# Kernel optimization log

Hardware: AMD Instinct MI355X
Metric: run time of the kernel (lower is better)

Reference implementation:

```python
import jax, jax.numpy as jnp
import numpy as np

N = 20000
NUM_CLASSES = 30


def setup_inputs() -> dict:
    key = jax.random.key(0)
    k1, k2, k3 = jax.random.split(key, 3)
    mean_3d = jax.random.normal(k1, (N, 3), dtype=jnp.float32)
    mean_3d_cano = jax.random.normal(k2, (N, 3), dtype=jnp.float32)
    segm_labels = jax.random.randint(k3, (N,), 0, NUM_CLASSES, dtype=jnp.int32)
    return {"mean_3d": mean_3d, "mean_3d_cano": mean_3d_cano, "segm_labels": segm_labels}


def reference(mean_3d, mean_3d_cano, segm_labels):
    # Brute-force K=1 nearest neighbor: squared euclidean distance
    # d2[i, j] = ||x_i||^2 - 2 x_i . y_j + ||y_j||^2  -> [N, N]
    x2 = jnp.sum(mean_3d * mean_3d, axis=-1, keepdims=True)          # [N, 1]
    y2 = jnp.sum(mean_3d_cano * mean_3d_cano, axis=-1)               # [N]
    d2 = x2 - 2.0 * (mean_3d @ mean_3d_cano.T) + y2[None, :]         # [N, N]
    nearest_ids = jnp.argmin(d2, axis=1)                              # [N]
    matched_labels = segm_labels[nearest_ids]
    semantic_inconsistent = (matched_labels != segm_labels)
    semantic_loss = semantic_inconsistent.astype(jnp.float32).mean()
    return semantic_loss
```

## Files before the change

### kernel.cpp

```cpp
#include <hip/hip_runtime.h>

#define N_PTS 20000
#define NA 20480
#define NB 20032
#define TILES_TOTAL 640
#define A_BYTES  (NA * 16 * 2)
#define B_BYTES  (NB * 16 * 2)
#define BEST_OFF (A_BYTES + B_BYTES)
#define CNT_OFF  (BEST_OFF + NB * 8)

typedef __attribute__((ext_vector_type(8))) short bf16x8;
typedef __attribute__((ext_vector_type(16))) float f32x16;

static __device__ __forceinline__ unsigned short f2bf(float f) {
    unsigned int u = __float_as_uint(f);
    unsigned int r = (u + 0x7FFFu + ((u >> 16) & 1u)) >> 16;
    return (unsigned short)r;
}
static __device__ __forceinline__ float bf2f(unsigned short h) {
    return __uint_as_float(((unsigned int)h) << 16);
}

static __device__ __forceinline__ unsigned long long packmin(float v, int idx) {
    unsigned u = __float_as_uint(v);
    u ^= (u & 0x80000000u) ? 0xFFFFFFFFu : 0x80000000u;
    return ((unsigned long long)u << 32) | (unsigned)idx;
}

__global__ __launch_bounds__(256) void nn_prep(const float* __restrict__ q,
                                               const float* __restrict__ c,
                                               unsigned short* __restrict__ Amat,
                                               unsigned short* __restrict__ Bmat,
                                               unsigned long long* __restrict__ best,
                                               unsigned int* __restrict__ counters) {
    const int m = blockIdx.x * 256 + (int)threadIdx.x;
    if (m < 2) counters[m] = 0u;
    if (m < NB) best[m] = 0xFFFFFFFFFFFFFFFFull;
    if (m < NA) {
        unsigned short a[16];
        #pragma unroll
        for (int r = 0; r < 16; ++r) a[r] = 0;
        if (m < N_PTS) {
            const float cx = c[m * 3 + 0], cy = c[m * 3 + 1], cz = c[m * 3 + 2];
            const unsigned short hx = f2bf(cx), hy = f2bf(cy), hz = f2bf(cz);
            const float lx = cx - bf2f(hx), ly = cy - bf2f(hy), lz = cz - bf2f(hz);
            const float y2 = fmaf(cx, cx, fmaf(cy, cy, cz * cz));
            const unsigned short y2h = f2bf(y2);
            const unsigned short y2l = f2bf(y2 - bf2f(y2h));
            a[0] = f2bf(-2.f * bf2f(hx)); a[1] = f2bf(-2.f * bf2f(hy)); a[2] = f2bf(-2.f * bf2f(hz));
            a[3] = a[0]; a[4] = a[1]; a[5] = a[2];
            a[6] = f2bf(-2.f * lx); a[7] = f2bf(-2.f * ly); a[8] = f2bf(-2.f * lz);
            a[9] = y2h; a[10] = y2l;
        } else {
            a[9] = f2bf(1e30f);
        }
        unsigned int* o = (unsigned int*)(Amat + (size_t)m * 16);
        #pragma unroll
        for (int r = 0; r < 8; ++r)
            o[r] = (unsigned int)a[2 * r] | ((unsigned int)a[2 * r + 1] << 16);
    }
    if (m < NB) {
        unsigned short b[16];
        #pragma unroll
        for (int r = 0; r < 16; ++r) b[r] = 0;
        if (m < N_PTS) {
            const float qx = q[m * 3 + 0], qy = q[m * 3 + 1], qz = q[m * 3 + 2];
            const unsigned short hx = f2bf(qx), hy = f2bf(qy), hz = f2bf(qz);
            b[0] = hx; b[1] = hy; b[2] = hz;
            b[3] = f2bf(qx - bf2f(hx)); b[4] = f2bf(qy - bf2f(hy)); b[5] = f2bf(qz - bf2f(hz));
            b[6] = hx; b[7] = hy; b[8] = hz;
            b[9] = f2bf(1.0f); b[10] = f2bf(1.0f);
        }
        unsigned int* o = (unsigned int*)(Bmat + (size_t)m * 16);
        #pragma unroll
        for (int r = 0; r < 8; ++r)
            o[r] = (unsigned int)b[2 * r] | ((unsigned int)b[2 * r + 1] << 16);
    }
}

static __device__ __forceinline__ float tree_min16(const f32x16& v) {
    const float t0 = fminf(fminf(v[0], v[1]), v[2]);
    const float t1 = fminf(fminf(v[3], v[4]), v[5]);
    const float t2 = fminf(fminf(v[6], v[7]), v[8]);
    const float t3 = fminf(fminf(v[9], v[10]), v[11]);
    const float t4 = fminf(fminf(v[12], v[13]), v[14]);
    const float t5 = fminf(fminf(t0, t1), v[15]);
    const float t6 = fminf(fminf(t2, t3), t4);
    return fminf(t5, t6);
}

static __device__ __forceinline__ int tile_argreg(const f32x16& v) {
    float pm = __uint_as_float(0x7F800000u);
    #pragma unroll
    for (int r = 0; r < 16; ++r)
        pm = fminf(pm, __uint_as_float((__float_as_uint(v[r]) & 0xFFFFFFF0u) | (unsigned)r));
    return (int)(__float_as_uint(pm) & 15u);
}

template<int LC>
__global__ __launch_bounds__(256, 2) void nn_main(const unsigned short* __restrict__ Amat,
                                                  const unsigned short* __restrict__ Bmat,
                                                  unsigned long long* __restrict__ best) {
    constexpr int C = 1 << LC;
    constexpr int TPC = TILES_TOTAL >> LC;

    const int wav = (int)(threadIdx.x >> 6);
    const int ch = blockIdx.x & (C - 1);
    const int qg = ((int)blockIdx.x >> LC) * 4 + wav;
    if (qg >= 313) return;
    const int lane = (int)(threadIdx.x & 63);
    const int qbase = qg * 64;
    const int l31 = lane & 31;
    const int half = lane >> 5;

    const bf16x8 b1 = *(const bf16x8*)(Bmat + (size_t)(qbase + l31) * 16 + half * 8);
    const bf16x8 b2 = *(const bf16x8*)(Bmat + (size_t)(qbase + 32 + l31) * 16 + half * 8);

    const f32x16 zacc = {0.f, 0.f, 0.f, 0.f, 0.f, 0.f, 0.f, 0.f,
                         0.f, 0.f, 0.f, 0.f, 0.f, 0.f, 0.f, 0.f};

    float bv1 = __uint_as_float(0x7F800000u), bv2 = bv1;
    int bp1 = 0, bp2 = 0;

    const unsigned short* Abase = Amat + ((size_t)(ch * TPC) * 32 + l31) * 16 + half * 8;
    const unsigned short* Ap = Abase;
    #pragma unroll 2
    for (int t = 0; t < TPC; ++t) {
        const bf16x8 af = *(const bf16x8*)Ap;
        Ap += 512;
        const f32x16 a1 = __builtin_amdgcn_mfma_f32_32x32x16_bf16(af, b1, zacc, 0, 0, 0);
        const float m1 = tree_min16(a1);
        if (m1 < bv1) bp1 = t;
        bv1 = fminf(bv1, m1);
        const f32x16 a2 = __builtin_amdgcn_mfma_f32_32x32x16_bf16(af, b2, zacc, 0, 0, 0);
        const float m2 = tree_min16(a2);
        if (m2 < bv2) bp2 = t;
        bv2 = fminf(bv2, m2);
    }

    int bi1, bi2;
    {
        const bf16x8 e1 = *(const bf16x8*)(Abase + (size_t)bp1 * 512);
        const f32x16 r1 = __builtin_amdgcn_mfma_f32_32x32x16_bf16(e1, b1, zacc, 0, 0, 0);
        const int rg1 = tile_argreg(r1);
        bi1 = (ch * TPC + bp1) * 32 + (rg1 & 3) + 8 * (rg1 >> 2) + 4 * half;
        const bf16x8 e2 = *(const bf16x8*)(Abase + (size_t)bp2 * 512);
        const f32x16 r2 = __builtin_amdgcn_mfma_f32_32x32x16_bf16(e2, b2, zacc, 0, 0, 0);
        const int rg2 = tile_argreg(r2);
        bi2 = (ch * TPC + bp2) * 32 + (rg2 & 3) + 8 * (rg2 >> 2) + 4 * half;
    }

    const float ov1 = __shfl_xor(bv1, 32);
    const int oi1 = __shfl_xor(bi1, 32);
    if (ov1 < bv1 || (ov1 == bv1 && oi1 < bi1)) { bv1 = ov1; bi1 = oi1; }
    const float ov2 = __shfl_xor(bv2, 32);
    const int oi2 = __shfl_xor(bi2, 32);
    if (ov2 < bv2 || (ov2 == bv2 && oi2 < bi2)) { bv2 = ov2; bi2 = oi2; }

    const unsigned long long pk = half ? packmin(bv2, bi2) : packmin(bv1, bi1);
    atomicMin(&best[qbase + lane], pk);
}

__global__ __launch_bounds__(256) void nn_final(const unsigned long long* __restrict__ best,
                                                const int* __restrict__ labels,
                                                unsigned int* __restrict__ count,
                                                unsigned int* __restrict__ ticket,
                                                float* __restrict__ out) {
    const int i = blockIdx.x * 256 + (int)threadIdx.x;
    int mism = 0;
    if (i < N_PTS) {
        int bidx = (int)(unsigned)(best[i] & 0xFFFFFFFFull);
        bidx = (bidx < 0) ? 0 : ((bidx >= N_PTS) ? (N_PTS - 1) : bidx);
        mism = (labels[bidx] != labels[i]) ? 1 : 0;
    }
    const unsigned long long msk = __ballot(mism != 0);
    __shared__ unsigned int bsum;
    if (threadIdx.x == 0) bsum = 0;
    __syncthreads();
    if ((threadIdx.x & 63) == 0) atomicAdd(&bsum, (unsigned)__popcll(msk));
    __syncthreads();
    if (threadIdx.x == 0) {
        atomicAdd(count, bsum);
        __threadfence();
        const unsigned t = atomicAdd(ticket, 1u);
        if (t == gridDim.x - 1) {
            __threadfence();
            const unsigned total = atomicAdd(count, 0u);
            out[0] = (float)total / (float)N_PTS;
        }
    }
}

extern "C" void kernel_launch(void* const* d_in, const int* in_sizes, int n_in,
                              void* d_out, int out_size, void* d_ws, size_t ws_size,
                              hipStream_t stream) {
    const float* mean_3d      = (const float*)d_in[0];
    const float* mean_3d_cano = (const float*)d_in[1];
    const int*   segm_labels  = (const int*)d_in[2];
    float* out = (float*)d_out;

    unsigned short* Amat = (unsigned short*)d_ws;
    unsigned short* Bmat = (unsigned short*)((char*)d_ws + A_BYTES);
    unsigned long long* best = (unsigned long long*)((char*)d_ws + BEST_OFF);
    unsigned int* counters = (unsigned int*)((char*)d_ws + CNT_OFF);

    constexpr int lc = 5;
    constexpr int C = 1 << lc;

    nn_prep<<<NA / 256, 256, 0, stream>>>(mean_3d, mean_3d_cano, Amat, Bmat, best, counters);
    nn_main<lc><<<C * 79, 256, 0, stream>>>(Amat, Bmat, best);
    nn_final<<<(N_PTS + 255) / 256, 256, 0, stream>>>(best, segm_labels, counters, counters + 1, out);
}
```

Before: 31.92 us.

## Fuse final label-mismatch reduction into main NN kernel via last-block ticket

Removes the separate nn_final launch. Every main block now takes a ticket after its atomicMin updates, and the last block to finish reads all best entries and counts label mismatches. This saves one kernel launch and its dependency gap. In exchange, the tail work (20000 points, strided loop) runs on a single block of 256 threads, which serialises part of the work.

```diff
diff --git a/kernel.cpp b/kernel.cpp
--- a/kernel.cpp
+++ b/kernel.cpp
@@ -100,94 +100,95 @@
 template<int LC>
 __global__ __launch_bounds__(256, 2) void nn_main(const unsigned short* __restrict__ Amat,
                                                   const unsigned short* __restrict__ Bmat,
-                                                  unsigned long long* __restrict__ best) {
+                                                  unsigned long long* __restrict__ best,
+                                                  const int* __restrict__ labels,
+                                                  unsigned int* __restrict__ ticket,
+                                                  float* __restrict__ out) {
     constexpr int C = 1 << LC;
     constexpr int TPC = TILES_TOTAL >> LC;
-
-    const int wav = (int)(threadIdx.x >> 6);
+    __shared__ unsigned int bsum;
+    __shared__ int islast;
+
+    const int tid = (int)threadIdx.x;
+    const int wav = tid >> 6;
     const int ch = blockIdx.x & (C - 1);
     const int qg = ((int)blockIdx.x >> LC) * 4 + wav;
-    if (qg >= 313) return;
-    const int lane = (int)(threadIdx.x & 63);
-    const int qbase = qg * 64;
+    const int lane = tid & 63;
     const int l31 = lane & 31;
     const int half = lane >> 5;
 
-    const bf16x8 b1 = *(const bf16x8*)(Bmat + (size_t)(qbase + l31) * 16 + half * 8);
-    const bf16x8 b2 = *(const bf16x8*)(Bmat + (size_t)(qbase + 32 + l31) * 16 + half * 8);
-
-    const f32x16 zacc = {0.f, 0.f, 0.f, 0.f, 0.f, 0.f, 0.f, 0.f,
-                         0.f, 0.f, 0.f, 0.f, 0.f, 0.f, 0.f, 0.f};
-
-    float bv1 = __uint_as_float(0x7F800000u), bv2 = bv1;
-    int bp1 = 0, bp2 = 0;
-
-    const unsigned short* Abase = Amat + ((size_t)(ch * TPC) * 32 + l31) * 16 + half * 8;
-    const unsigned short* Ap = Abase;
-    #pragma unroll 2
-    for (int t = 0; t < TPC; ++t) {
-        const bf16x8 af = *(const bf16x8*)Ap;
-        Ap += 512;
-        const f32x16 a1 = __builtin_amdgcn_mfma_f32_32x32x16_bf16(af, b1, zacc, 0, 0, 0);
-        const float m1 = tree_min16(a1);
-        if (m1 < bv1) bp1 = t;
-        bv1 = fminf(bv1, m1);
-        const f32x16 a2 = __builtin_amdgcn_mfma_f32_32x32x16_bf16(af, b2, zacc, 0, 0, 0);
-        const float m2 = tree_min16(a2);
-        if (m2 < bv2) bp2 = t;
-        bv2 = fminf(bv2, m2);
-    }
-
-    int bi1, bi2;
-    {
-        const bf16x8 e1 = *(const bf16x8*)(Abase + (size_t)bp1 * 512);
-        const f32x16 r1 = __builtin_amdgcn_mfma_f32_32x32x16_bf16(e1, b1, zacc, 0, 0, 0);
-        const int rg1 = tile_argreg(r1);
-        bi1 = (ch * TPC + bp1) * 32 + (rg1 & 3) + 8 * (rg1 >> 2) + 4 * half;
-        const bf16x8 e2 = *(const bf16x8*)(Abase + (size_t)bp2 * 512);
-        const f32x16 r2 = __builtin_amdgcn_mfma_f32_32x32x16_bf16(e2, b2, zacc, 0, 0, 0);
-        const int rg2 = tile_argreg(r2);
-        bi2 = (ch * TPC + bp2) * 32 + (rg2 & 3) + 8 * (rg2 >> 2) + 4 * half;
-    }
-
-    const float ov1 = __shfl_xor(bv1, 32);
-    const int oi1 = __shfl_xor(bi1, 32);
-    if (ov1 < bv1 || (ov1 == bv1 && oi1 < bi1)) { bv1 = ov1; bi1 = oi1; }
-    const float ov2 = __shfl_xor(bv2, 32);
-    const int oi2 = __shfl_xor(bi2, 32);
-    if (ov2 < bv2 || (ov2 == bv2 && oi2 < bi2)) { bv2 = ov2; bi2 = oi2; }
-
-    const unsigned long long pk = half ? packmin(bv2, bi2) : packmin(bv1, bi1);
-    atomicMin(&best[qbase + lane], pk);
-}
-
-__global__ __launch_bounds__(256) void nn_final(const unsigned long long* __restrict__ best,
-                                                const int* __restrict__ labels,
-                                                unsigned int* __restrict__ count,
-                                                unsigned int* __restrict__ ticket,
-                                                float* __restrict__ out) {
-    const int i = blockIdx.x * 256 + (int)threadIdx.x;
-    int mism = 0;
-    if (i < N_PTS) {
-        int bidx = (int)(unsigned)(best[i] & 0xFFFFFFFFull);
-        bidx = (bidx < 0) ? 0 : ((bidx >= N_PTS) ? (N_PTS - 1) : bidx);
-        mism = (labels[bidx] != labels[i]) ? 1 : 0;
-    }
-    const unsigned long long msk = __ballot(mism != 0);
-    __shared__ unsigned int bsum;
-    if (threadIdx.x == 0) bsum = 0;
+    if (qg < 313) {
+        const int qbase = qg * 64;
+        const bf16x8 b1 = *(const bf16x8*)(Bmat + (size_t)(qbase + l31) * 16 + half * 8);
+        const bf16x8 b2 = *(const bf16x8*)(Bmat + (size_t)(qbase + 32 + l31) * 16 + half * 8);
+
+        const f32x16 zacc = {0.f, 0.f, 0.f, 0.f, 0.f, 0.f, 0.f, 0.f,
+                             0.f, 0.f, 0.f, 0.f, 0.f, 0.f, 0.f, 0.f};
+
+        float bv1 = __uint_as_float(0x7F800000u), bv2 = bv1;
+        int bp1 = 0, bp2 = 0;
+
+        const unsigned short* Abase = Amat + ((size_t)(ch * TPC) * 32 + l31) * 16 + half * 8;
+        const unsigned short* Ap = Abase;
+        #pragma unroll 2
+        for (int t = 0; t < TPC; ++t) {
+            const bf16x8 af = *(const bf16x8*)Ap;
+            Ap += 512;
+            const f32x16 a1 = __builtin_amdgcn_mfma_f32_32x32x16_bf16(af, b1, zacc, 0, 0, 0);
+            const float m1 = tree_min16(a1);
+            if (m1 < bv1) bp1 = t;
+            bv1 = fminf(bv1, m1);
+            const f32x16 a2 = __builtin_amdgcn_mfma_f32_32x32x16_bf16(af, b2, zacc, 0, 0, 0);
+            const float m2 = tree_min16(a2);
+            if (m2 < bv2) bp2 = t;
+            bv2 = fminf(bv2, m2);
+        }
+
+        int bi1, bi2;
+        {
+            const bf16x8 e1 = *(const bf16x8*)(Abase + (size_t)bp1 * 512);
+            const f32x16 r1 = __builtin_amdgcn_mfma_f32_32x32x16_bf16(e1, b1, zacc, 0, 0, 0);
+            const int rg1 = tile_argreg(r1);
+            bi1 = (ch * TPC + bp1) * 32 + (rg1 & 3) + 8 * (rg1 >> 2) + 4 * half;
+            const bf16x8 e2 = *(const bf16x8*)(Abase + (size_t)bp2 * 512);
+            const f32x16 r2 = __builtin_amdgcn_mfma_f32_32x32x16_bf16(e2, b2, zacc, 0, 0, 0);
+            const int rg2 = tile_argreg(r2);
+            bi2 = (ch * TPC + bp2) * 32 + (rg2 & 3) + 8 * (rg2 >> 2) + 4 * half;
+        }
+
+        const float ov1 = __shfl_xor(bv1, 32);
+        const int oi1 = __shfl_xor(bi1, 32);
+        if (ov1 < bv1 || (ov1 == bv1 && oi1 < bi1)) { bv1 = ov1; bi1 = oi1; }
+        const float ov2 = __shfl_xor(bv2, 32);
+        const int oi2 = __shfl_xor(bi2, 32);
+        if (ov2 < bv2 || (ov2 == bv2 && oi2 < bi2)) { bv2 = ov2; bi2 = oi2; }
+
+        const unsigned long long pk = half ? packmin(bv2, bi2) : packmin(bv1, bi1);
+        atomicMin(&best[qbase + lane], pk);
+    }
+
     __syncthreads();
-    if ((threadIdx.x & 63) == 0) atomicAdd(&bsum, (unsigned)__popcll(msk));
+    if (tid == 0) {
+        __threadfence();
+        islast = (atomicAdd(ticket, 1u) == (unsigned)gridDim.x - 1u) ? 1 : 0;
+        bsum = 0u;
+    }
     __syncthreads();
-    if (threadIdx.x == 0) {
-        atomicAdd(count, bsum);
-        __threadfence();
-        const unsigned t = atomicAdd(ticket, 1u);
-        if (t == gridDim.x - 1) {
-            __threadfence();
-            const unsigned total = atomicAdd(count, 0u);
-            out[0] = (float)total / (float)N_PTS;
-        }
+
+    if (islast) {
+        unsigned cnt = 0;
+        for (int i = tid; i < N_PTS; i += 256) {
+            const unsigned long long b =
+                __hip_atomic_load(&best[i], __ATOMIC_RELAXED, __HIP_MEMORY_SCOPE_AGENT);
+            int bidx = (int)(unsigned)(b & 0xFFFFFFFFull);
+            bidx = (bidx < 0) ? 0 : ((bidx >= N_PTS) ? (N_PTS - 1) : bidx);
+            cnt += (labels[bidx] != labels[i]) ? 1u : 0u;
+        }
+        #pragma unroll
+        for (int off = 32; off > 0; off >>= 1) cnt += __shfl_down(cnt, off);
+        if ((tid & 63) == 0) atomicAdd(&bsum, cnt);
+        __syncthreads();
+        if (tid == 0) out[0] = (float)bsum / (float)N_PTS;
     }
 }
 
@@ -208,6 +209,5 @@
     constexpr int C = 1 << lc;
 
     nn_prep<<<NA / 256, 256, 0, stream>>>(mean_3d, mean_3d_cano, Amat, Bmat, best, counters);
-    nn_main<lc><<<C * 79, 256, 0, stream>>>(Amat, Bmat, best);
-    nn_final<<<(N_PTS + 255) / 256, 256, 0, stream>>>(best, segm_labels, counters, counters + 1, out);
-}
+    nn_main<lc><<<C * 79, 256, 0, stream>>>(Amat, Bmat, best, segm_labels, counters + 1, out);
+}
```

Result: slower. 89.59 us (+180.6%).
